# Kernel tuning notes

Measured on AMD Instinct MI355X. Metric: run time of the kernel, lower is better.

The kernel has to match this reference:

```python
import jax, jax.numpy as jnp
import numpy as np

B, T, N, S = 128, 1024, 128, 256
NEG = jnp.float32(-1e30)  # acts as -inf but keeps grads finite


def setup_inputs() -> dict:
    key = jax.random.key(0)
    k1, k2, k3, k4, k5 = jax.random.split(key, 5)
    inputs = jax.random.normal(k1, (B, T, N), dtype=jnp.float32)
    # nn.Parameter inits to zeros; use small noise so transition actually participates
    transition = 0.05 * jax.random.normal(k2, (N, N), dtype=jnp.float32)
    targets = jax.random.randint(k3, (B, S), 0, N)
    input_lengths = jax.random.randint(k4, (B,), T // 2, T + 1).astype(jnp.int32)
    target_lengths = jax.random.randint(k5, (B,), S // 2, S + 1).astype(jnp.int32)
    return {
        "transition": transition,
        "inputs": inputs,
        "targets": targets,
        "input_lengths": input_lengths,
        "target_lengths": target_lengths,
    }


def reference(transition, inputs, targets, input_lengths, target_lengths):
    # ASG loss = FCC (free-running partition) - FAC (forced alignment score),
    # scale_mode='none', reduction='mean'. transition[j, i] = score of label i -> j.
    xs = jnp.moveaxis(inputs, 1, 0)  # (T, B, N)
    ts = jnp.arange(1, T)

    # ---- FCC: alpha[t, b, j] = x[t,b,j] + logsumexp_i(alpha[t-1,b,i] + trans[j,i])
    def fcc_step(alpha, xt):
        x_t, t = xt
        new = x_t + jax.nn.logsumexp(alpha[:, None, :] + transition[None, :, :], axis=-1)
        return jnp.where((t < input_lengths)[:, None], new, alpha), None

    alphaT, _ = jax.lax.scan(fcc_step, xs[0], (xs[1:], ts))
    fcc = jax.nn.logsumexp(alphaT, axis=-1)  # (B,)

    # ---- FAC: beta[t, b, s] over target positions, self/next transitions only
    self_tr = transition[targets, targets]  # (B, S): stay on targets[s]
    prev_lbl = jnp.concatenate([targets[:, :1], targets[:, :-1]], axis=1)
    next_tr = transition[targets, prev_lbl]  # (B, S): targets[s-1] -> targets[s]

    em0 = jnp.take_along_axis(xs[0], targets, axis=1)  # (B, S)
    beta0 = jnp.where(jnp.arange(S)[None, :] == 0, em0, NEG)

    def fac_step(beta, xt):
        x_t, t = xt
        em = jnp.take_along_axis(x_t, targets, axis=1)  # (B, S)
        shifted = jnp.concatenate(
            [jnp.full((B, 1), NEG, dtype=beta.dtype), beta[:, :-1]], axis=1
        )
        new = em + jnp.logaddexp(beta + self_tr, shifted + next_tr)
        return jnp.where((t < input_lengths)[:, None], new, beta), None

    betaT, _ = jax.lax.scan(fac_step, beta0, (xs[1:], ts))
    fac = jnp.take_along_axis(betaT, (target_lengths - 1)[:, None], axis=1)[:, 0]

    return jnp.mean(fcc - fac)
```

## Files before the change

kernel.cpp:

```cpp
#include <hip/hip_runtime.h>
#include <hip/hip_bf16.h>

#define Bb 128
#define Tt 1024
#define Nn 128
#define Ss 256
#define NEGF (-1e30f)
#define D9 9.0f

typedef __attribute__((ext_vector_type(8))) short short8;
typedef __attribute__((ext_vector_type(4))) float f32x4;

__device__ __forceinline__ short bf16b(float f) {
    __hip_bfloat16 h = __float2bfloat16(f);
    return *reinterpret_cast<short*>(&h);
}

__device__ __forceinline__ unsigned int cvt_pk_bf16(float lo, float hi) {
    unsigned int r;
    asm("v_cvt_pk_bf16_f32 %0, %1, %2" : "=v"(r) : "v"(lo), "v"(hi));
    return r;
}

#define LDS_BARRIER() asm volatile("s_waitcnt lgkmcnt(0)\n\ts_barrier" ::: "memory")

#define FCC_STEP(t_, k_)                                                       \
    {                                                                          \
        const int t = (t_);                                                    \
        const int sl = (k_) & 3;                   \
                            \
        short8 bfA = *(const short8*)(rp[(t - 1) & 1][0]);                     \
        short8 bfB = *(const short8*)(rp[(t - 1) & 1][1]);                     \
        short8 bfC = *(const short8*)(rp[(t - 1) & 1][2]);                     \
               \
        const f32x4 zz = {0.f, 0.f, 0.f, 0.f};                                 \
        f32x4 p1_0 = __builtin_amdgcn_mfma_f32_16x16x32_bf16(e_own0, bf_own, zz, 0, 0, 0); \
        f32x4 p1_1 = __builtin_amdgcn_mfma_f32_16x16x32_bf16(e_own1, bf_own, zz, 0, 0, 0); \
        f32x4 w0 = xs[sl][0], w1 = xs[sl][1];                                  \
        if (!PRE) {                                                            \
            w0[0] = __expf(w0[0] - D9); w0[1] = __expf(w0[1] - D9);            \
            w0[2] = __expf(w0[2] - D9); w0[3] = __expf(w0[3] - D9);            \
            w1[0] = __expf(w1[0] - D9); w1[1] = __expf(w1[1] - D9);            \
            w1[2] = __expf(w1[2] - D9); w1[3] = __expf(w1[3] - D9);            \
        }                                                                      \
        {     \
            int tn = t + 4; if (tn > Tt - 1) tn = Tt - 1;                      \
            const float* gb = wbase + (size_t)tn * TSTR;                       \
            xs[sl][0] = *(const f32x4*)(gb);                                   \
            xs[sl][1] = *(const f32x4*)(gb + MSTR);                            \
        }                                                                      \
        if ((k_) == 0) { \
            float m = fmaxf(fmaxf(wred[0][g], wred[1][g]),                     \
                            fmaxf(wred[2][g], wred[3][g]));                    \
            float invm = 1.0f / m;                                             \
            c += __logf(m);                                                    \
            w0 *= invm; w1 *= invm;                                            \
        }                                                                      \
                  \
        p1_0 = __builtin_amdgcn_mfma_f32_16x16x32_bf16(eoA0, bfA, p1_0, 0, 0, 0); \
        p1_1 = __builtin_amdgcn_mfma_f32_16x16x32_bf16(eoA1, bfA, p1_1, 0, 0, 0); \
        f32x4 p2_0 = __builtin_amdgcn_mfma_f32_16x16x32_bf16(eoB0, bfB, zz, 0, 0, 0); \
        f32x4 p2_1 = __builtin_amdgcn_mfma_f32_16x16x32_bf16(eoB1, bfB, zz, 0, 0, 0); \
        f32x4 p3_0 = __builtin_amdgcn_mfma_f32_16x16x32_bf16(eoC0, bfC, zz, 0, 0, 0); \
        f32x4 p3_1 = __builtin_amdgcn_mfma_f32_16x16x32_bf16(eoC1, bfC, zz, 0, 0, 0); \
        f32x4 un0 = w0 * ((p1_0 + p2_0) + p3_0);                               \
        f32x4 un1 = w1 * ((p1_1 + p2_1) + p3_1);                               \
        if (t == len - 1) {  \
            float s = (un0[0] + un0[1]) + (un0[2] + un0[3])                    \
                    + (un1[0] + un1[1]) + (un1[2] + un1[3]);                   \
            s += __shfl_xor(s, 16);                                            \
            s += __shfl_xor(s, 32);                                            \
            sfin = s; cfin = c;                                                \
        }                                                                      \
        uint2 o0, o1;                                                          \
        o0.x = cvt_pk_bf16(un0[0], un0[1]); o0.y = cvt_pk_bf16(un0[2], un0[3]); \
        o1.x = cvt_pk_bf16(un1[0], un1[1]); o1.y = cvt_pk_bf16(un1[2], un1[3]); \
        {  \
           \
           \
            unsigned sx = lowhalf ? o0.x : o1.x;                               \
            unsigned sy = lowhalf ? o0.y : o1.y;                               \
            union { short8 s8; int i4[4]; } BO;                                \
            BO.i4[0] = __builtin_amdgcn_ds_bpermute(addrA, (int)sx);           \
            BO.i4[1] = __builtin_amdgcn_ds_bpermute(addrA, (int)sy);           \
            BO.i4[2] = __builtin_amdgcn_ds_bpermute(addrB, (int)sx);           \
            BO.i4[3] = __builtin_amdgcn_ds_bpermute(addrB, (int)sy);           \
            bf_own = BO.s8;                                                    \
        }                                                                      \
        *reinterpret_cast<uint2*>(wp[t & 1]) = o0;                             \
        *reinterpret_cast<uint2*>(wp[t & 1] + 16) = o1;                        \
        if ((k_) == 7) { \
            float mm = fmaxf(fmaxf(un0[0], un0[1]), fmaxf(un0[2], un0[3]));    \
            mm = fmaxf(mm, fmaxf(fmaxf(un1[0], un1[1]), fmaxf(un1[2], un1[3])));\
            mm = fmaxf(mm, __shfl_xor(mm, 16));                                \
            mm = fmaxf(mm, __shfl_xor(mm, 32));                                \
            if (lane < 16) wred[q][lane] = mm;                                 \
        }                                                                      \
        LDS_BARRIER();                                                         \
    }

#define FAC_STEP(t_, k_)                                                       \
    {                                                                          \
        const int t = (t_);                                                    \
        const int d = ((k_) + 7) & 7;                                          \
        float e0 = em[d][0], e1 = em[d][1], e2 = em[d][2], e3 = em[d][3];      \
        int tn = t + 8; if (tn > Tt - 1) tn = Tt - 1;                          \
        const float* xrow = xb + (size_t)tn * Nn;                              \
        em[d][0] = xrow[tgi[0]]; em[d][1] = xrow[tgi[1]];                      \
        em[d][2] = xrow[tgi[2]]; em[d][3] = xrow[tgi[3]];                      \
        float bup = __shfl_up(bt[3], 1);                                       \
        float prev0 = (lane == 0) ? NEGF : bup;                                \
        float nb[4];                                                           \
        {                                                                      \
            float aa = bt[0] + st[0], bb = prev0 + ntr[0];                     \
            float hi = fmaxf(aa, bb), lo = fminf(aa, bb);                      \
            nb[0] = e0 + hi + __logf(1.0f + __expf(lo - hi));                  \
        }                                                                      \
        {                                                                      \
            float aa = bt[1] + st[1], bb = bt[0] + ntr[1];                     \
            float hi = fmaxf(aa, bb), lo = fminf(aa, bb);                      \
            nb[1] = e1 + hi + __logf(1.0f + __expf(lo - hi));                  \
        }                                                                      \
        {                                                                      \
            float aa = bt[2] + st[2], bb = bt[1] + ntr[2];                     \
            float hi = fmaxf(aa, bb), lo = fminf(aa, bb);                      \
            nb[2] = e2 + hi + __logf(1.0f + __expf(lo - hi));                  \
        }                                                                      \
        {                                                                      \
            float aa = bt[3] + st[3], bb = bt[2] + ntr[3];                     \
            float hi = fmaxf(aa, bb), lo = fminf(aa, bb);                      \
            nb[3] = e3 + hi + __logf(1.0f + __expf(lo - hi));                  \
        }                                                                      \
        if (t < len) {                                                         \
            bt[0] = nb[0]; bt[1] = nb[1]; bt[2] = nb[2]; bt[3] = nb[3];        \
        }                                                                      \
    }

__global__ __launch_bounds__(256) void exp_w_kernel(const float* __restrict__ x,
                                                    float* __restrict__ w) {
    const int nf4 = Bb * Tt * Nn / 4;
    const int stride = gridDim.x * 256;
    for (int f = blockIdx.x * 256 + threadIdx.x; f < nf4; f += stride) {
        const int l    = f & 63;
        const int mt   = (f >> 6) & 1;
        const int qq   = (f >> 7) & 3;
        const int wv   = (f >> 9) & 7;
        const int t    = f >> 12;
        const int b    = (wv << 4) + (l & 15);
        const int j    = (qq << 5) + (mt << 4) + ((l >> 4) << 2);
        f32x4 v = *(const f32x4*)(x + ((size_t)b * Tt + t) * Nn + j);
        f32x4 r;
        r[0] = __expf(v[0] - D9); r[1] = __expf(v[1] - D9);
        r[2] = __expf(v[2] - D9); r[3] = __expf(v[3] - D9);
        *(f32x4*)(w + 4 * (size_t)f) = r;
    }
}

template <bool PRE>
__global__ __launch_bounds__(256, 1) void asg_main(
    const float* __restrict__ trans, const float* __restrict__ x,
    const float* __restrict__ Wm,
    const int* __restrict__ targets, const int* __restrict__ ilen,
    const int* __restrict__ tlen,
    float* __restrict__ fcc_out, float* __restrict__ fac_out)
{
    __shared__ __align__(16) short ut[2][16][136];
    __shared__ float wred[4][16];

    const int tid  = threadIdx.x;
    const int q    = tid >> 6;
    const int lane = tid & 63;

    if (blockIdx.x < 8) {
        const int g    = lane & 15;
        const int quad = lane >> 4;
        const int wv   = blockIdx.x;
        const int b    = (wv << 4) + g;
        const int len  = ilen[b];

        constexpr int TSTR = PRE ? 16384 : Nn;
        constexpr int MSTR = PRE ? 64 * 4 : 16;
        const float* wbase = PRE
            ? (Wm + (size_t)(((wv << 2) + q) << 1) * 256 + (lane << 2))
            : (x + (size_t)b * (Tt * Nn) + 32 * q + 4 * quad);

        short8 ea[2][4];
        #pragma unroll
        for (int mt = 0; mt < 2; ++mt) {
            const float* tr = trans + (size_t)(32 * q + 16 * mt + g) * Nn + quad * 8;
            #pragma unroll
            for (int kc = 0; kc < 4; ++kc) {
                short8 v;
                #pragma unroll
                for (int jj = 0; jj < 8; ++jj)
                    v[jj] = bf16b(__expf(tr[kc * 32 + jj]));
                ea[mt][kc] = v;
            }
        }

        short8 e_own0, e_own1, eoA0, eoA1, eoB0, eoB1, eoC0, eoC1;
        int oc0, oc1, oc2;
        if (q == 0) {
            e_own0 = ea[0][0]; e_own1 = ea[1][0];
            eoA0 = ea[0][1]; eoA1 = ea[1][1];
            eoB0 = ea[0][2]; eoB1 = ea[1][2];
            eoC0 = ea[0][3]; eoC1 = ea[1][3];
            oc0 = 32; oc1 = 64; oc2 = 96;
        } else if (q == 1) {
            e_own0 = ea[0][1]; e_own1 = ea[1][1];
            eoA0 = ea[0][0]; eoA1 = ea[1][0];
            eoB0 = ea[0][2]; eoB1 = ea[1][2];
            eoC0 = ea[0][3]; eoC1 = ea[1][3];
            oc0 = 0; oc1 = 64; oc2 = 96;
        } else if (q == 2) {
            e_own0 = ea[0][2]; e_own1 = ea[1][2];
            eoA0 = ea[0][0]; eoA1 = ea[1][0];
            eoB0 = ea[0][1]; eoB1 = ea[1][1];
            eoC0 = ea[0][3]; eoC1 = ea[1][3];
            oc0 = 0; oc1 = 32; oc2 = 96;
        } else {
            e_own0 = ea[0][3]; e_own1 = ea[1][3];
            eoA0 = ea[0][0]; eoA1 = ea[1][0];
            eoB0 = ea[0][1]; eoB1 = ea[1][1];
            eoC0 = ea[0][2]; eoC1 = ea[1][2];
            oc0 = 0; oc1 = 32; oc2 = 64;
        }

        const short* rp[2][3];
        short* wp[2];
        {
            const short* b0 = &ut[0][g][quad * 8];
            const short* b1 = &ut[1][g][quad * 8];
            rp[0][0] = b0 + oc0; rp[0][1] = b0 + oc1; rp[0][2] = b0 + oc2;
            rp[1][0] = b1 + oc0; rp[1][1] = b1 + oc1; rp[1][2] = b1 + oc2;
            wp[0] = &ut[0][g][32 * q + 4 * quad];
            wp[1] = &ut[1][g][32 * q + 4 * quad];
        }
        const int  addrA   = ((quad & 1) * 32 + g) * 4;
        const int  addrB   = addrA + 64;
        const bool lowhalf = (quad < 2);

        f32x4 xs[4][2];
        short8 bf_own;
        float c = 0.f, sfin = 1.0f, cfin = 0.f;

        {
            f32x4 v0 = *(const f32x4*)(wbase);
            f32x4 v1 = *(const f32x4*)(wbase + MSTR);
            if (!PRE) {
                v0[0]=__expf(v0[0]-D9); v0[1]=__expf(v0[1]-D9);
                v0[2]=__expf(v0[2]-D9); v0[3]=__expf(v0[3]-D9);
                v1[0]=__expf(v1[0]-D9); v1[1]=__expf(v1[1]-D9);
                v1[2]=__expf(v1[2]-D9); v1[3]=__expf(v1[3]-D9);
            }
            uint2 o0, o1;
            o0.x = cvt_pk_bf16(v0[0], v0[1]); o0.y = cvt_pk_bf16(v0[2], v0[3]);
            o1.x = cvt_pk_bf16(v1[0], v1[1]); o1.y = cvt_pk_bf16(v1[2], v1[3]);
            {
                unsigned sx = lowhalf ? o0.x : o1.x;
                unsigned sy = lowhalf ? o0.y : o1.y;
                union { short8 s8; int i4[4]; } BO;
                BO.i4[0] = __builtin_amdgcn_ds_bpermute(addrA, (int)sx);
                BO.i4[1] = __builtin_amdgcn_ds_bpermute(addrA, (int)sy);
                BO.i4[2] = __builtin_amdgcn_ds_bpermute(addrB, (int)sx);
                BO.i4[3] = __builtin_amdgcn_ds_bpermute(addrB, (int)sy);
                bf_own = BO.s8;
            }
            *reinterpret_cast<uint2*>(wp[0]) = o0;
            *reinterpret_cast<uint2*>(wp[0] + 16) = o1;
        }
        #pragma unroll
        for (int k = 1; k <= 4; ++k) {
            const float* rr = wbase + (size_t)k * TSTR;
            xs[k & 3][0] = *(const f32x4*)(rr);
            xs[k & 3][1] = *(const f32x4*)(rr + MSTR);
        }
        __syncthreads();

        #pragma unroll
        for (int k = 1; k < 8; ++k) FCC_STEP(k, k)
        for (int tb = 8; tb < Tt; tb += 8) {
            #pragma unroll
            for (int k = 0; k < 8; ++k) FCC_STEP(tb + k, k)
        }

        if (lane < 16) wred[q][lane] = sfin;
        __syncthreads();
        if (q == 0 && lane < 16) {
            float tot = wred[0][lane] + wred[1][lane] + wred[2][lane] + wred[3][lane];
            fcc_out[(wv << 4) + lane] = cfin + D9 * (float)len + __logf(tot);
        }
    } else {
        const int b   = ((blockIdx.x - 8) << 2) + q;
        const int len = ilen[b];
        const int tl  = tlen[b];
        const float* xb = x + (size_t)b * Tt * Nn;

        int   tgi[4];
        float st[4], ntr[4], bt[4];
        #pragma unroll
        for (int r = 0; r < 4; ++r) {
            const int s = (lane << 2) + r;
            const int tgv = targets[b * Ss + s];
            const int pg  = (s == 0) ? tgv : targets[b * Ss + s - 1];
            tgi[r] = tgv;
            st[r]  = trans[tgv * Nn + tgv];
            ntr[r] = trans[tgv * Nn + pg];
            bt[r]  = (s == 0) ? xb[tgv] : NEGF;
        }
        float em[8][4];
        #pragma unroll
        for (int k = 1; k <= 8; ++k) {
            int tt = k; if (tt > Tt - 1) tt = Tt - 1;
            const float* xrow = xb + (size_t)tt * Nn;
            em[(k - 1) & 7][0] = xrow[tgi[0]];
            em[(k - 1) & 7][1] = xrow[tgi[1]];
            em[(k - 1) & 7][2] = xrow[tgi[2]];
            em[(k - 1) & 7][3] = xrow[tgi[3]];
        }

        #pragma unroll
        for (int k = 1; k < 8; ++k) FAC_STEP(k, k)
        for (int tb = 8; tb < Tt; tb += 8) {
            #pragma unroll
            for (int k = 0; k < 8; ++k) FAC_STEP(tb + k, k)
        }

        #pragma unroll
        for (int r = 0; r < 4; ++r)
            if ((lane << 2) + r == tl - 1) fac_out[b] = bt[r];
    }
}

__global__ __launch_bounds__(128) void reduce_kernel(const float* __restrict__ fcc,
                                                     const float* __restrict__ fac,
                                                     float* __restrict__ out) {
    __shared__ float r2[2];
    int tid = threadIdx.x;
    float v = fcc[tid] - fac[tid];
    #pragma unroll
    for (int o = 32; o > 0; o >>= 1) v += __shfl_xor(v, o);
    if ((tid & 63) == 0) r2[tid >> 6] = v;
    __syncthreads();
    if (tid == 0) out[0] = (r2[0] + r2[1]) * (1.0f / Bb);
}

extern "C" void kernel_launch(void* const* d_in, const int* in_sizes, int n_in,
                              void* d_out, int out_size, void* d_ws, size_t ws_size,
                              hipStream_t stream) {
    const float* trans   = (const float*)d_in[0];
    const float* x       = (const float*)d_in[1];
    const int*   targets = (const int*)d_in[2];
    const int*   ilen    = (const int*)d_in[3];
    const int*   tlen    = (const int*)d_in[4];
    float* out = (float*)d_out;

    float* fcc = (float*)d_ws;
    float* fac = fcc + Bb;
    float* Wm  = (float*)((char*)d_ws + 2048);

    const size_t wbytes = (size_t)Bb * Tt * Nn * sizeof(float);
    const bool pre = ws_size >= wbytes + 2048;

    if (pre) {
        exp_w_kernel<<<2048, 256, 0, stream>>>(x, Wm);
        asg_main<true><<<40, 256, 0, stream>>>(trans, x, Wm, targets, ilen, tlen, fcc, fac);
    } else {
        asg_main<false><<<40, 256, 0, stream>>>(trans, x, x, targets, ilen, tlen, fcc, fac);
    }
    reduce_kernel<<<1, 128, 0, stream>>>(fcc, fac, out);
}
```

Baseline: 457.7 us.

## Permute label ordering so MFMA output matches B-operand layout, dropping bpermute

Reorders the mapping of labels to MFMA rows (transition rows, x/W loads, LDS write offsets) so that each lane's MFMA output fragment is directly usable as its own B-operand. This removes the four ds_bpermute ops per step and replaces two 8-byte LDS stores with one 16-byte store. It also chains the B and C partial MFMAs into one accumulator to cut vector adds. Ping-pong buffer indices are now computed from the unroll index instead of t. The risk is that the permuted layout must stay consistent across the precompute kernel and the recurrence.

```diff
diff --git a/kernel.cpp b/kernel.cpp
--- a/kernel.cpp
+++ b/kernel.cpp
@@ -27,15 +27,16 @@
 #define FCC_STEP(t_, k_)                                                       \
     {                                                                          \
         const int t = (t_);                                                    \
-        const int sl = (k_) & 3;                   \
-                            \
-        short8 bfA = *(const short8*)(rp[(t - 1) & 1][0]);                     \
-        short8 bfB = *(const short8*)(rp[(t - 1) & 1][1]);                     \
-        short8 bfC = *(const short8*)(rp[(t - 1) & 1][2]);                     \
-               \
+        const int sl  = (k_) & 3;                  \
+        const int RPp = ((k_) & 1) ^ 1;            \
+        const int WPp = (k_) & 1;                      \
+        short8 bfA = *(const short8*)(rp[RPp][0]);                             \
+        short8 bfB = *(const short8*)(rp[RPp][1]);                             \
+        short8 bfC = *(const short8*)(rp[RPp][2]);                             \
         const f32x4 zz = {0.f, 0.f, 0.f, 0.f};                                 \
-        f32x4 p1_0 = __builtin_amdgcn_mfma_f32_16x16x32_bf16(e_own0, bf_own, zz, 0, 0, 0); \
-        f32x4 p1_1 = __builtin_amdgcn_mfma_f32_16x16x32_bf16(e_own1, bf_own, zz, 0, 0, 0); \
+        \
+        f32x4 c1_0 = __builtin_amdgcn_mfma_f32_16x16x32_bf16(e_own0, bf_own, zz, 0, 0, 0); \
+        f32x4 c1_1 = __builtin_amdgcn_mfma_f32_16x16x32_bf16(e_own1, bf_own, zz, 0, 0, 0); \
         f32x4 w0 = xs[sl][0], w1 = xs[sl][1];                                  \
         if (!PRE) {                                                            \
             w0[0] = __expf(w0[0] - D9); w0[1] = __expf(w0[1] - D9);            \
@@ -56,15 +57,14 @@
             c += __logf(m);                                                    \
             w0 *= invm; w1 *= invm;                                            \
         }                                                                      \
-                  \
-        p1_0 = __builtin_amdgcn_mfma_f32_16x16x32_bf16(eoA0, bfA, p1_0, 0, 0, 0); \
-        p1_1 = __builtin_amdgcn_mfma_f32_16x16x32_bf16(eoA1, bfA, p1_1, 0, 0, 0); \
-        f32x4 p2_0 = __builtin_amdgcn_mfma_f32_16x16x32_bf16(eoB0, bfB, zz, 0, 0, 0); \
-        f32x4 p2_1 = __builtin_amdgcn_mfma_f32_16x16x32_bf16(eoB1, bfB, zz, 0, 0, 0); \
-        f32x4 p3_0 = __builtin_amdgcn_mfma_f32_16x16x32_bf16(eoC0, bfC, zz, 0, 0, 0); \
-        f32x4 p3_1 = __builtin_amdgcn_mfma_f32_16x16x32_bf16(eoC1, bfC, zz, 0, 0, 0); \
-        f32x4 un0 = w0 * ((p1_0 + p2_0) + p3_0);                               \
-        f32x4 un1 = w1 * ((p1_1 + p2_1) + p3_1);                               \
+        c1_0 = __builtin_amdgcn_mfma_f32_16x16x32_bf16(eoA0, bfA, c1_0, 0, 0, 0); \
+        c1_1 = __builtin_amdgcn_mfma_f32_16x16x32_bf16(eoA1, bfA, c1_1, 0, 0, 0); \
+        f32x4 c2_0 = __builtin_amdgcn_mfma_f32_16x16x32_bf16(eoB0, bfB, zz, 0, 0, 0); \
+        f32x4 c2_1 = __builtin_amdgcn_mfma_f32_16x16x32_bf16(eoB1, bfB, zz, 0, 0, 0); \
+        c2_0 = __builtin_amdgcn_mfma_f32_16x16x32_bf16(eoC0, bfC, c2_0, 0, 0, 0); \
+        c2_1 = __builtin_amdgcn_mfma_f32_16x16x32_bf16(eoC1, bfC, c2_1, 0, 0, 0); \
+        f32x4 un0 = w0 * (c1_0 + c2_0);                                        \
+        f32x4 un1 = w1 * (c1_1 + c2_1);                                        \
         if (t == len - 1) {  \
             float s = (un0[0] + un0[1]) + (un0[2] + un0[3])                    \
                     + (un1[0] + un1[1]) + (un1[2] + un1[3]);                   \
@@ -72,23 +72,15 @@
             s += __shfl_xor(s, 32);                                            \
             sfin = s; cfin = c;                                                \
         }                                                                      \
-        uint2 o0, o1;                                                          \
-        o0.x = cvt_pk_bf16(un0[0], un0[1]); o0.y = cvt_pk_bf16(un0[2], un0[3]); \
-        o1.x = cvt_pk_bf16(un1[0], un1[1]); o1.y = cvt_pk_bf16(un1[2], un1[3]); \
-        {  \
-           \
-           \
-            unsigned sx = lowhalf ? o0.x : o1.x;                               \
-            unsigned sy = lowhalf ? o0.y : o1.y;                               \
-            union { short8 s8; int i4[4]; } BO;                                \
-            BO.i4[0] = __builtin_amdgcn_ds_bpermute(addrA, (int)sx);           \
-            BO.i4[1] = __builtin_amdgcn_ds_bpermute(addrA, (int)sy);           \
-            BO.i4[2] = __builtin_amdgcn_ds_bpermute(addrB, (int)sx);           \
-            BO.i4[3] = __builtin_amdgcn_ds_bpermute(addrB, (int)sy);           \
-            bf_own = BO.s8;                                                    \
-        }                                                                      \
-        *reinterpret_cast<uint2*>(wp[t & 1]) = o0;                             \
-        *reinterpret_cast<uint2*>(wp[t & 1] + 16) = o1;                        \
+        {                                                                      \
+            union { short8 s8; unsigned u[4]; } OW;                            \
+            OW.u[0] = cvt_pk_bf16(un0[0], un0[1]);                             \
+            OW.u[1] = cvt_pk_bf16(un0[2], un0[3]);                             \
+            OW.u[2] = cvt_pk_bf16(un1[0], un1[1]);                             \
+            OW.u[3] = cvt_pk_bf16(un1[2], un1[3]);                             \
+            *reinterpret_cast<short8*>(wptr[WPp]) = OW.s8;        \
+            bf_own = OW.s8;       \
+        }                                                                      \
         if ((k_) == 7) { \
             float mm = fmaxf(fmaxf(un0[0], un0[1]), fmaxf(un0[2], un0[3]));    \
             mm = fmaxf(mm, fmaxf(fmaxf(un1[0], un1[1]), fmaxf(un1[2], un1[3])));\
@@ -142,12 +134,12 @@
     const int stride = gridDim.x * 256;
     for (int f = blockIdx.x * 256 + threadIdx.x; f < nf4; f += stride) {
         const int l    = f & 63;
-        const int mt   = (f >> 6) & 1;
+        const int half = (f >> 6) & 1;
         const int qq   = (f >> 7) & 3;
         const int wv   = (f >> 9) & 7;
         const int t    = f >> 12;
         const int b    = (wv << 4) + (l & 15);
-        const int j    = (qq << 5) + (mt << 4) + ((l >> 4) << 2);
+        const int j    = (qq << 5) + ((l >> 4) << 3) + (half << 2);
         f32x4 v = *(const f32x4*)(x + ((size_t)b * Tt + t) * Nn + j);
         f32x4 r;
         r[0] = __expf(v[0] - D9); r[1] = __expf(v[1] - D9);
@@ -179,15 +171,16 @@
         const int len  = ilen[b];
 
         constexpr int TSTR = PRE ? 16384 : Nn;
-        constexpr int MSTR = PRE ? 64 * 4 : 16;
+        constexpr int MSTR = PRE ? 256 : 4;
         const float* wbase = PRE
-            ? (Wm + (size_t)(((wv << 2) + q) << 1) * 256 + (lane << 2))
-            : (x + (size_t)b * (Tt * Nn) + 32 * q + 4 * quad);
+            ? (Wm + (size_t)((wv << 3) + (q << 1)) * 256 + (lane << 2))
+            : (x + (size_t)b * (Tt * Nn) + 32 * q + 8 * quad);
 
         short8 ea[2][4];
         #pragma unroll
         for (int mt = 0; mt < 2; ++mt) {
-            const float* tr = trans + (size_t)(32 * q + 16 * mt + g) * Nn + quad * 8;
+            const int srow = 32 * q + 8 * (g >> 2) + 4 * mt + (g & 3);
+            const float* tr = trans + (size_t)srow * Nn + quad * 8;
             #pragma unroll
             for (int kc = 0; kc < 4; ++kc) {
                 short8 v;
@@ -227,18 +220,15 @@
         }
 
         const short* rp[2][3];
-        short* wp[2];
+        short* wptr[2];
         {
-            const short* b0 = &ut[0][g][quad * 8];
-            const short* b1 = &ut[1][g][quad * 8];
+            const short* b0 = &ut[0][g][8 * quad];
+            const short* b1 = &ut[1][g][8 * quad];
             rp[0][0] = b0 + oc0; rp[0][1] = b0 + oc1; rp[0][2] = b0 + oc2;
             rp[1][0] = b1 + oc0; rp[1][1] = b1 + oc1; rp[1][2] = b1 + oc2;
-            wp[0] = &ut[0][g][32 * q + 4 * quad];
-            wp[1] = &ut[1][g][32 * q + 4 * quad];
-        }
-        const int  addrA   = ((quad & 1) * 32 + g) * 4;
-        const int  addrB   = addrA + 64;
-        const bool lowhalf = (quad < 2);
+            wptr[0] = &ut[0][g][32 * q + 8 * quad];
+            wptr[1] = &ut[1][g][32 * q + 8 * quad];
+        }
 
         f32x4 xs[4][2];
         short8 bf_own;
@@ -253,21 +243,13 @@
                 v1[0]=__expf(v1[0]-D9); v1[1]=__expf(v1[1]-D9);
                 v1[2]=__expf(v1[2]-D9); v1[3]=__expf(v1[3]-D9);
             }
-            uint2 o0, o1;
-            o0.x = cvt_pk_bf16(v0[0], v0[1]); o0.y = cvt_pk_bf16(v0[2], v0[3]);
-            o1.x = cvt_pk_bf16(v1[0], v1[1]); o1.y = cvt_pk_bf16(v1[2], v1[3]);
-            {
-                unsigned sx = lowhalf ? o0.x : o1.x;
-                unsigned sy = lowhalf ? o0.y : o1.y;
-                union { short8 s8; int i4[4]; } BO;
-                BO.i4[0] = __builtin_amdgcn_ds_bpermute(addrA, (int)sx);
-                BO.i4[1] = __builtin_amdgcn_ds_bpermute(addrA, (int)sy);
-                BO.i4[2] = __builtin_amdgcn_ds_bpermute(addrB, (int)sx);
-                BO.i4[3] = __builtin_amdgcn_ds_bpermute(addrB, (int)sy);
-                bf_own = BO.s8;
-            }
-            *reinterpret_cast<uint2*>(wp[0]) = o0;
-            *reinterpret_cast<uint2*>(wp[0] + 16) = o1;
+            union { short8 s8; unsigned u[4]; } OW;
+            OW.u[0] = cvt_pk_bf16(v0[0], v0[1]);
+            OW.u[1] = cvt_pk_bf16(v0[2], v0[3]);
+            OW.u[2] = cvt_pk_bf16(v1[0], v1[1]);
+            OW.u[3] = cvt_pk_bf16(v1[2], v1[3]);
+            *reinterpret_cast<short8*>(wptr[0]) = OW.s8;
+            bf_own = OW.s8;
         }
         #pragma unroll
         for (int k = 1; k <= 4; ++k) {
```

Result: faster. 378.7 us (-17.2%).
